# Kernel tuning notes

Measured on AMD Instinct MI355X. Metric: run time of the kernel, lower is better.

Reference implementation:

```python
import jax, jax.numpy as jnp
import numpy as np

B, S, R = 1, 128, 384          # batch, n_seq (MSA rows), n_res
C_M, C_Z, H, D = 256, 128, 8, 32  # msa channels, pair channels, heads, head dim


def layernorm(x, g, b, eps=1e-5):
    mu = jnp.mean(x, axis=-1, keepdims=True)
    var = jnp.var(x, axis=-1, keepdims=True)
    return (x - mu) * jax.lax.rsqrt(var + eps) * g + b


def setup_inputs() -> dict:
    key = jax.random.key(0)
    ks = jax.random.split(key, 10)
    w = lambda k, shape: jax.random.normal(k, shape, jnp.float32) * 0.02
    return {
        "msa_act": jax.random.normal(ks[0], (B, S, R, C_M), jnp.float32),
        "pair_act": jax.random.normal(ks[1], (B, R, R, C_Z), jnp.float32),
        "msa_mask": jnp.ones((B, S, R), jnp.float32),
        "qn_g": jnp.ones((C_M,), jnp.float32),
        "qn_b": jnp.zeros((C_M,), jnp.float32),
        "pn_g": jnp.ones((C_Z,), jnp.float32),
        "pn_b": jnp.zeros((C_Z,), jnp.float32),
        "w_pair": w(ks[2], (C_Z, H)),           # feat_2d_weights (no bias)
        "wq": w(ks[3], (C_M, H, D)),
        "wk": w(ks[4], (C_M, H, D)),
        "wv": w(ks[5], (C_M, H, D)),
        "wg": w(ks[6], (C_M, H, D)),            # gating linear
        "bg": jnp.ones((H, D), jnp.float32),     # gating bias (AF2 inits to 1)
        "wo": w(ks[7], (H, D, C_M)),             # output projection
        "bo": jnp.zeros((C_M,), jnp.float32),
    }


def reference(msa_act, pair_act, msa_mask, qn_g, qn_b, pn_g, pn_b,
              w_pair, wq, wk, wv, wg, bg, wo, bo):
    # pair bias: LN + Linear(c_z -> H), -> [B, 1, H, R, R]
    z = jnp.einsum('bijc,ch->bhij', layernorm(pair_act, pn_g, pn_b), w_pair)[:, None]
    # mask bias: [B, S, 1, 1, R]
    mask_bias = (1e9 * (msa_mask - 1.0))[:, :, None, None, :]

    m = layernorm(msa_act, qn_g, qn_b)
    q = jnp.einsum('bsrc,chd->bshrd', m, wq) * (D ** -0.5)
    k = jnp.einsum('bsrc,chd->bshrd', m, wk)
    v = jnp.einsum('bsrc,chd->bshrd', m, wv)

    logits = jnp.einsum('bshqd,bshkd->bshqk', q, k) + mask_bias + z  # [B,S,H,R,R]
    a = jax.nn.softmax(logits, axis=-1)
    o = jnp.einsum('bshqk,bshkd->bsqhd', a, v)                       # [B,S,R,H,D]

    g = jax.nn.sigmoid(jnp.einsum('bsrc,chd->bsrhd', m, wg) + bg)
    out = jnp.einsum('bsrhd,hdc->bsrc', o * g, wo) + bo              # [B,S,R,C_M]
    return out
```

## Files before the change

### kernel.cpp

```cpp
#include <hip/hip_runtime.h>
#include <hip/hip_bf16.h>

typedef unsigned int uint;
typedef unsigned short ushortT;
typedef __attribute__((ext_vector_type(8))) short bf16x8;
typedef __attribute__((ext_vector_type(4))) float f32x4;

#define S_ 128
#define R_ 384
#define CM 256
#define CZ 128
#define H_ 8
#define D_ 32
#define SR (S_*R_)
#define RRTOT (R_*R_)
#define SHRD (S_*H_*R_*D_)

__device__ __forceinline__ float bf2f(ushortT u) {
    return __uint_as_float(((uint)u) << 16);
}
__device__ __forceinline__ ushortT f2bf(float f) {
    uint x = __float_as_uint(f);
    x += 0x7FFFu + ((x >> 16) & 1u);
    return (ushortT)(x >> 16);
}
__device__ __forceinline__ uint pack_bf2(float lo, float hi) {
    return (uint)f2bf(lo) | ((uint)f2bf(hi) << 16);
}

__global__ __launch_bounds__(256) void k_prep(
        const float* __restrict__ wq, const float* __restrict__ wk,
        const float* __restrict__ wv, const float* __restrict__ wg,
        const float* __restrict__ wo,
        ushortT* __restrict__ wt, ushortT* __restrict__ wgt,
        ushortT* __restrict__ wot) {
    int id = blockIdx.x * 256 + threadIdx.x;
    int which = id >> 16, r16 = id & 65535;
    int y = r16 & 255, x = r16 >> 8;
    if (which == 0)      wt[(size_t)y*256 + x]       = f2bf(wq[(size_t)x*256 + y] * 0.17677669529663687f);
    else if (which == 1) wt[(size_t)(256+y)*256 + x] = f2bf(wk[(size_t)x*256 + y]);
    else if (which == 2) wt[(size_t)(512+y)*256 + x] = f2bf(wv[(size_t)x*256 + y]);
    else if (which == 3) wgt[(size_t)y*256 + x]      = f2bf(wg[(size_t)x*256 + y]);
    else                 wot[(size_t)y*256 + x]      = f2bf(wo[(size_t)x*256 + y]);
}

__global__ __launch_bounds__(256) void k_pair_bias(
        const float* __restrict__ pair, const float* __restrict__ pn_g,
        const float* __restrict__ pn_b, const float* __restrict__ w_pair,
        ushortT* __restrict__ z) {
    int wave = threadIdx.x >> 6, lane = threadIdx.x & 63;
    int row = blockIdx.x * 4 + wave;
    const float* x = pair + (size_t)row * CZ;
    float2 xv = *(const float2*)&x[lane * 2];
    float s  = xv.x + xv.y;
    float s2 = xv.x*xv.x + xv.y*xv.y;
    #pragma unroll
    for (int off = 32; off; off >>= 1) {
        s  += __shfl_xor(s,  off);
        s2 += __shfl_xor(s2, off);
    }
    float mu  = s * (1.0f / 128.0f);
    float var = s2 * (1.0f / 128.0f) - mu * mu;
    float rstd = rsqrtf(var + 1e-5f);
    float2 gv = *(const float2*)&pn_g[lane * 2];
    float2 bv = *(const float2*)&pn_b[lane * 2];
    float n0 = (xv.x - mu) * rstd * gv.x + bv.x;
    float n1 = (xv.y - mu) * rstd * gv.y + bv.y;
    float4 wa = *(const float4*)&w_pair[lane*16     ];
    float4 wb = *(const float4*)&w_pair[lane*16 +  4];
    float4 wc = *(const float4*)&w_pair[lane*16 +  8];
    float4 wd = *(const float4*)&w_pair[lane*16 + 12];
    float v0_ = n0*wa.x + n1*wc.x, v1_ = n0*wa.y + n1*wc.y;
    float v2_ = n0*wa.z + n1*wc.z, v3_ = n0*wa.w + n1*wc.w;
    float v4_ = n0*wb.x + n1*wd.x, v5_ = n0*wb.y + n1*wd.y;
    float v6_ = n0*wb.z + n1*wd.z, v7_ = n0*wb.w + n1*wd.w;
    float x0 = __shfl_xor(v0_,1), x1 = __shfl_xor(v1_,1), x2 = __shfl_xor(v2_,1), x3 = __shfl_xor(v3_,1);
    float x4 = __shfl_xor(v4_,1), x5 = __shfl_xor(v5_,1), x6 = __shfl_xor(v6_,1), x7 = __shfl_xor(v7_,1);
    bool b0 = (lane & 1) != 0;
    float u0 = b0 ? v4_+x4 : v0_+x0;
    float u1 = b0 ? v5_+x5 : v1_+x1;
    float u2 = b0 ? v6_+x6 : v2_+x2;
    float u3 = b0 ? v7_+x7 : v3_+x3;
    float y0 = __shfl_xor(u0,2), y1 = __shfl_xor(u1,2), y2 = __shfl_xor(u2,2), y3 = __shfl_xor(u3,2);
    bool b1 = (lane & 2) != 0;
    float w0 = b1 ? u2+y2 : u0+y0;
    float w1 = b1 ? u3+y3 : u1+y1;
    float z0 = __shfl_xor(w0,4), z1 = __shfl_xor(w1,4);
    bool b2 = (lane & 4) != 0;
    float val = b2 ? w1+z1 : w0+z0;
    val += __shfl_xor(val, 8);
    val += __shfl_xor(val, 16);
    val += __shfl_xor(val, 32);
    int hmap = 4*(lane & 1) + 2*((lane >> 1) & 1) + ((lane >> 2) & 1);
    if (lane < 8) z[(size_t)hmap * RRTOT + row] = f2bf(val);
}

__device__ __forceinline__ void ln_row_f4(
        const float* __restrict__ src, const float* __restrict__ gam,
        const float* __restrict__ bet, char* msb, int row, int lane) {
    float4 xv = *(const float4*)&src[lane * 4];
    float sm = (xv.x + xv.y) + (xv.z + xv.w);
    float s2 = (xv.x*xv.x + xv.y*xv.y) + (xv.z*xv.z + xv.w*xv.w);
    #pragma unroll
    for (int off = 32; off; off >>= 1) {
        sm += __shfl_xor(sm, off);
        s2 += __shfl_xor(s2, off);
    }
    float mu  = sm * (1.0f / 256.0f);
    float var = s2 * (1.0f / 256.0f) - mu * mu;
    float rstd = rsqrtf(var + 1e-5f);
    float4 gv = *(const float4*)&gam[lane * 4];
    float4 bv = *(const float4*)&bet[lane * 4];
    float n0 = (xv.x - mu) * rstd * gv.x + bv.x, n1 = (xv.y - mu) * rstd * gv.y + bv.y;
    float n2 = (xv.z - mu) * rstd * gv.z + bv.z, n3 = (xv.w - mu) * rstd * gv.w + bv.w;
    uint2 w; w.x = pack_bf2(n0, n1); w.y = pack_bf2(n2, n3);
    *(uint2*)(msb + ((row*512 + lane*8) ^ ((row & 7) << 4))) = w;
}

__global__ __launch_bounds__(256) void k_msa_qkv(
        const float* __restrict__ msa, const float* __restrict__ qn_g,
        const float* __restrict__ qn_b, const ushortT* __restrict__ wt,
        ushortT* __restrict__ qo, ushortT* __restrict__ ko,
        ushortT* __restrict__ vto) {
    __shared__ ushortT m_sh[32 * 256];
    __shared__ ushortT st_sh[3 * 32 * 256];
    int tid = threadIdx.x, wave = tid >> 6, lane = tid & 63;
    int c = lane & 15, g = (lane >> 4) & 3;
    int r0 = blockIdx.x * 32, s = r0 / R_, rl0 = r0 % R_;
    char* msb = (char*)m_sh;
    char* stb = (char*)st_sh;

    #pragma unroll
    for (int i = 0; i < 8; ++i) {
        int row = wave * 8 + i;
        ln_row_f4(msa + (size_t)(r0 + row) * CM, qn_g, qn_b, msb, row, lane);
    }
    __syncthreads();

    bf16x8 af[2][8];
    #pragma unroll
    for (int rt = 0; rt < 2; ++rt)
        #pragma unroll
        for (int kc = 0; kc < 8; ++kc) {
            int row = rt*16 + c;
            af[rt][kc] = *(const bf16x8*)(msb + ((row*512 + (kc*32 + 8*g)*2) ^ ((c & 7) << 4)));
        }

    const f32x4 z4 = {0.f, 0.f, 0.f, 0.f};
    #pragma unroll
    for (int mI = 0; mI < 3; ++mI) {
        char* osb = stb + mI * 16384;
        int tb = wave * 4;
        const ushortT* wb0 = wt + ((size_t)(mI*256 + tb*16 + c)) * 256 + 8*g;
        const ushortT* wb1 = wb0 + 16*256;
        const ushortT* wb2 = wb0 + 32*256;
        const ushortT* wb3 = wb0 + 48*256;
        f32x4 a0L = z4, a0H = z4, a1L = z4, a1H = z4;
        f32x4 a2L = z4, a2H = z4, a3L = z4, a3H = z4;
        #pragma unroll
        for (int kc = 0; kc < 8; ++kc) {
            bf16x8 b0 = *(const bf16x8*)(wb0 + kc*32);
            bf16x8 b1 = *(const bf16x8*)(wb1 + kc*32);
            bf16x8 b2 = *(const bf16x8*)(wb2 + kc*32);
            bf16x8 b3 = *(const bf16x8*)(wb3 + kc*32);
            a0L = __builtin_amdgcn_mfma_f32_16x16x32_bf16(af[0][kc], b0, a0L, 0, 0, 0);
            a0H = __builtin_amdgcn_mfma_f32_16x16x32_bf16(af[1][kc], b0, a0H, 0, 0, 0);
            a1L = __builtin_amdgcn_mfma_f32_16x16x32_bf16(af[0][kc], b1, a1L, 0, 0, 0);
            a1H = __builtin_amdgcn_mfma_f32_16x16x32_bf16(af[1][kc], b1, a1H, 0, 0, 0);
            a2L = __builtin_amdgcn_mfma_f32_16x16x32_bf16(af[0][kc], b2, a2L, 0, 0, 0);
            a2H = __builtin_amdgcn_mfma_f32_16x16x32_bf16(af[1][kc], b2, a2H, 0, 0, 0);
            a3L = __builtin_amdgcn_mfma_f32_16x16x32_bf16(af[0][kc], b3, a3L, 0, 0, 0);
            a3H = __builtin_amdgcn_mfma_f32_16x16x32_bf16(af[1][kc], b3, a3H, 0, 0, 0);
        }
        #pragma unroll
        for (int j = 0; j < 4; ++j) {
            f32x4 lo = (j == 0) ? a0L : (j == 1) ? a1L : (j == 2) ? a2L : a3L;
            f32x4 hi = (j == 0) ? a0H : (j == 1) ? a1H : (j == 2) ? a2H : a3H;
            if (mI < 2) {
                int col = (tb + j)*16 + c;
                #pragma unroll
                for (int r = 0; r < 4; ++r) {
                    int row0 = 4*g + r, row1 = row0 + 16;
                    *(ushortT*)(osb + ((row0*512 + col*2) ^ ((row0 & 7) << 4))) = f2bf(lo[r]);
                    *(ushortT*)(osb + ((row1*512 + col*2) ^ ((row1 & 7) << 4))) = f2bf(hi[r]);
                }
            } else {
                int hd = (tb + j)*16 + c;
                #pragma unroll
                for (int r = 0; r < 4; ++r) {
                    int rlo = 4*g + r, rhi = rlo + 16;
                    *(ushortT*)(osb + ((hd*64 + rlo*2) ^ ((hd & 3) << 4))) = f2bf(lo[r]);
                    *(ushortT*)(osb + ((hd*64 + rhi*2) ^ ((hd & 3) << 4))) = f2bf(hi[r]);
                }
            }
        }
    }
    __syncthreads();

    #pragma unroll
    for (int m = 0; m < 2; ++m) {
        char* osb = stb + m * 16384;
        ushortT* O = (m == 0) ? qo : ko;
        #pragma unroll
        for (int i = 0; i < 4; ++i) {
            int idx = tid + i*256;
            int row = idx >> 5, c16 = idx & 31;
            uint4 vd = *(const uint4*)(osb + ((row*512 + c16*16) ^ ((row & 7) << 4)));
            int hh = c16 >> 2, dq = (c16 & 3) * 8;
            size_t ga = ((size_t)(s*H_ + hh) * R_ + rl0 + row) * D_ + dq;
            *(uint4*)&O[ga] = vd;
        }
    }
    {
        char* osb = stb + 2 * 16384;
        #pragma unroll
        for (int i = 0; i < 4; ++i) {
            int idx = tid + i*256;
            int hd = idx >> 2, q8 = idx & 3;
            uint4 vd = *(const uint4*)(osb + ((hd*64 + q8*16) ^ ((hd & 3) << 4)));
            size_t ga = ((size_t)(s*256 + hd)) * R_ + rl0 + q8*8;
            *(uint4*)&vto[ga] = vd;
        }
    }
}

__global__ __launch_bounds__(512) void k_attn(
        const ushortT* __restrict__ qws, const ushortT* __restrict__ kws,
        const ushortT* __restrict__ vtws, const ushortT* __restrict__ zws,
        const float* __restrict__ mask, float* __restrict__ out) {
    __shared__ ushortT k_sh[R_ * 40];
    __shared__ ushortT vt_sh[D_ * R_];
    __shared__ float   mb[R_];
    __shared__ ushortT p_sh[8 * 1280];
    int tid = threadIdx.x, wave = tid >> 6, lane = tid & 63;
    int c = lane & 15, g = (lane >> 4) & 3;
    int s = blockIdx.x >> 3, h = blockIdx.x & 7;
    size_t base = (size_t)(s * H_ + h) * R_ * D_;

    {
        const uint4* ks = (const uint4*)(kws + base);
        char* kb_ = (char*)k_sh;
        for (int i = tid; i < 1536; i += 512) {
            int row = i >> 2, part = i & 3;
            *(uint4*)(kb_ + row*80 + part*16) = ks[i];
        }
        const uint4* vs = (const uint4*)(vtws + base);
        char* vb = (char*)vt_sh;
        for (int i = tid; i < 1536; i += 512) {
            int d = i / 48, ch = i % 48;
            *(uint4*)(vb + ((d*768 + ch*16) ^ ((d & 7) << 4))) = vs[i];
        }
        for (int j = tid; j < R_; j += 512) mb[j] = 1e9f * (mask[s*R_ + j] - 1.0f);
    }
    __syncthreads();

    const char* ksb = (const char*)k_sh;
    const char* vtb = (const char*)vt_sh;
    char* psb = (char*)p_sh + wave * 2560;
    const f32x4 zero4 = {0.f, 0.f, 0.f, 0.f};

    for (int qt = wave; qt < 24; qt += 8) {
        int q0 = qt * 16;
        bf16x8 qf = *(const bf16x8*)(qws + base + (size_t)(q0 + c) * D_ + 8*g);
        const ushortT* zq = zws + (size_t)h * RRTOT + (size_t)(q0 + c) * R_ + 4*g;

        float sm = 0.f;
        f32x4 o0 = zero4, o1 = zero4;
        #pragma unroll 2
        for (int kb = 0; kb < 12; ++kb) {
            bf16x8 kfA = *(const bf16x8*)(ksb + ((2*kb    )*16 + c)*80 + 16*g);
            bf16x8 kfB = *(const bf16x8*)(ksb + ((2*kb + 1)*16 + c)*80 + 16*g);
            f32x4 pA = __builtin_amdgcn_mfma_f32_16x16x32_bf16(kfA, qf, zero4, 0, 0, 0);
            f32x4 pB = __builtin_amdgcn_mfma_f32_16x16x32_bf16(kfB, qf, zero4, 0, 0, 0);
            float4 mvA = *(const float4*)&mb[(2*kb    )*16 + 4*g];
            float4 mvB = *(const float4*)&mb[(2*kb + 1)*16 + 4*g];
            ushort4 zvA = *(const ushort4*)(zq + (2*kb    )*16);
            ushort4 zvB = *(const ushort4*)(zq + (2*kb + 1)*16);
            pA.x = __expf(pA.x + mvA.x + bf2f(zvA.x));
            pA.y = __expf(pA.y + mvA.y + bf2f(zvA.y));
            pA.z = __expf(pA.z + mvA.z + bf2f(zvA.z));
            pA.w = __expf(pA.w + mvA.w + bf2f(zvA.w));
            pB.x = __expf(pB.x + mvB.x + bf2f(zvB.x));
            pB.y = __expf(pB.y + mvB.y + bf2f(zvB.y));
            pB.z = __expf(pB.z + mvB.z + bf2f(zvB.z));
            pB.w = __expf(pB.w + mvB.w + bf2f(zvB.w));
            sm += (pA.x + pA.y) + (pA.z + pA.w) + (pB.x + pB.y) + (pB.z + pB.w);
            uint2 wA; wA.x = pack_bf2(pA.x, pA.y); wA.y = pack_bf2(pA.z, pA.w);
            uint2 wB; wB.x = pack_bf2(pB.x, pB.y); wB.y = pack_bf2(pB.z, pB.w);
            *(uint2*)(psb + (kb&1)*1280 + c*80 +      8*g) = wA;
            *(uint2*)(psb + (kb&1)*1280 + c*80 + 32 + 8*g) = wB;
            bf16x8 pa = *(const bf16x8*)(psb + (kb&1)*1280 + c*80 + 16*g);
            bf16x8 v0 = *(const bf16x8*)(vtb + (((c     )*768 + kb*64 + 16*g) ^ ((c & 7) << 4)));
            bf16x8 v1 = *(const bf16x8*)(vtb + (((16 + c)*768 + kb*64 + 16*g) ^ ((c & 7) << 4)));
            o0 = __builtin_amdgcn_mfma_f32_16x16x32_bf16(v0, pa, o0, 0, 0, 0);
            o1 = __builtin_amdgcn_mfma_f32_16x16x32_bf16(v1, pa, o1, 0, 0, 0);
        }
        sm += __shfl_xor(sm, 16);
        sm += __shfl_xor(sm, 32);
        float inv = 1.0f / sm;
        float4 s0, s1;
        s0.x = o0[0]*inv; s0.y = o0[1]*inv; s0.z = o0[2]*inv; s0.w = o0[3]*inv;
        s1.x = o1[0]*inv; s1.y = o1[1]*inv; s1.z = o1[2]*inv; s1.w = o1[3]*inv;
        float* ob = out + (size_t)(s*R_ + q0 + c) * CM + h*D_ + 4*g;
        *(float4*)ob = s0;
        *(float4*)(ob + 16) = s1;
    }
}

__global__ __launch_bounds__(256) void k_out(
        const float* __restrict__ msa, const float* __restrict__ qn_g,
        const float* __restrict__ qn_b, const ushortT* __restrict__ wgt,
        const float* __restrict__ bg, const ushortT* __restrict__ wot,
        const float* __restrict__ bo, float* __restrict__ out) {
    __shared__ ushortT m_sh[32 * 256];
    __shared__ ushortT og_sh[32 * 256];
    int tid = threadIdx.x, wave = tid >> 6, lane = tid & 63;
    int c = lane & 15, g = (lane >> 4) & 3;
    int r0 = blockIdx.x * 32;
    char* msb = (char*)m_sh;
    char* ogb = (char*)og_sh;

    #pragma unroll
    for (int i = 0; i < 8; ++i) {
        int row = wave * 8 + i;
        ln_row_f4(msa + (size_t)(r0 + row) * CM, qn_g, qn_b, msb, row, lane);
    }
    __syncthreads();

    bf16x8 af[2][8];
    #pragma unroll
    for (int rt = 0; rt < 2; ++rt)
        #pragma unroll
        for (int kc = 0; kc < 8; ++kc) {
            int row = rt*16 + c;
            af[rt][kc] = *(const bf16x8*)(msb + ((row*512 + (kc*32 + 8*g)*2) ^ ((c & 7) << 4)));
        }

    const f32x4 z4 = {0.f, 0.f, 0.f, 0.f};
    {
        int tb = wave * 4;
        const ushortT* wb0 = wgt + (size_t)(tb*16 + c) * 256 + 8*g;
        const ushortT* wb1 = wb0 + 16*256;
        const ushortT* wb2 = wb0 + 32*256;
        const ushortT* wb3 = wb0 + 48*256;
        f32x4 a0L = z4, a0H = z4, a1L = z4, a1H = z4;
        f32x4 a2L = z4, a2H = z4, a3L = z4, a3H = z4;
        #pragma unroll
        for (int kc = 0; kc < 8; ++kc) {
            bf16x8 b0 = *(const bf16x8*)(wb0 + kc*32);
            bf16x8 b1 = *(const bf16x8*)(wb1 + kc*32);
            bf16x8 b2 = *(const bf16x8*)(wb2 + kc*32);
            bf16x8 b3 = *(const bf16x8*)(wb3 + kc*32);
            a0L = __builtin_amdgcn_mfma_f32_16x16x32_bf16(af[0][kc], b0, a0L, 0, 0, 0);
            a0H = __builtin_amdgcn_mfma_f32_16x16x32_bf16(af[1][kc], b0, a0H, 0, 0, 0);
            a1L = __builtin_amdgcn_mfma_f32_16x16x32_bf16(af[0][kc], b1, a1L, 0, 0, 0);
            a1H = __builtin_amdgcn_mfma_f32_16x16x32_bf16(af[1][kc], b1, a1H, 0, 0, 0);
            a2L = __builtin_amdgcn_mfma_f32_16x16x32_bf16(af[0][kc], b2, a2L, 0, 0, 0);
            a2H = __builtin_amdgcn_mfma_f32_16x16x32_bf16(af[1][kc], b2, a2H, 0, 0, 0);
            a3L = __builtin_amdgcn_mfma_f32_16x16x32_bf16(af[0][kc], b3, a3L, 0, 0, 0);
            a3H = __builtin_amdgcn_mfma_f32_16x16x32_bf16(af[1][kc], b3, a3H, 0, 0, 0);
        }
        #pragma unroll
        for (int j = 0; j < 4; ++j) {
            f32x4 lo = (j == 0) ? a0L : (j == 1) ? a1L : (j == 2) ? a2L : a3L;
            f32x4 hi = (j == 0) ? a0H : (j == 1) ? a1H : (j == 2) ? a2H : a3H;
            int t = (tb + j)*16 + c;
            float bgv = bg[t];
            #pragma unroll
            for (int r = 0; r < 4; ++r) {
                int row0 = 4*g + r, row1 = row0 + 16;
                float g0 = 1.0f / (1.0f + __expf(-(lo[r] + bgv)));
                float g1 = 1.0f / (1.0f + __expf(-(hi[r] + bgv)));
                float ov0 = out[(size_t)(r0 + row0) * CM + t];
                float ov1 = out[(size_t)(r0 + row1) * CM + t];
                *(ushortT*)(ogb + ((row0*512 + t*2) ^ ((row0 & 7) << 4))) = f2bf(ov0 * g0);
                *(ushortT*)(ogb + ((row1*512 + t*2) ^ ((row1 & 7) << 4))) = f2bf(ov1 * g1);
            }
        }
    }
    __syncthreads();

    bf16x8 af2[2][8];
    #pragma unroll
    for (int rt = 0; rt < 2; ++rt)
        #pragma unroll
        for (int kc = 0; kc < 8; ++kc) {
            int row = rt*16 + c;
            af2[rt][kc] = *(const bf16x8*)(ogb + ((row*512 + (kc*32 + 8*g)*2) ^ ((c & 7) << 4)));
        }

    {
        int tb = wave * 4;
        const ushortT* wb0 = wot + (size_t)(tb*16 + c) * 256 + 8*g;
        const ushortT* wb1 = wb0 + 16*256;
        const ushortT* wb2 = wb0 + 32*256;
        const ushortT* wb3 = wb0 + 48*256;
        f32x4 a0L = z4, a0H = z4, a1L = z4, a1H = z4;
        f32x4 a2L = z4, a2H = z4, a3L = z4, a3H = z4;
        #pragma unroll
        for (int kc = 0; kc < 8; ++kc) {
            bf16x8 b0 = *(const bf16x8*)(wb0 + kc*32);
            bf16x8 b1 = *(const bf16x8*)(wb1 + kc*32);
            bf16x8 b2 = *(const bf16x8*)(wb2 + kc*32);
            bf16x8 b3 = *(const bf16x8*)(wb3 + kc*32);
            a0L = __builtin_amdgcn_mfma_f32_16x16x32_bf16(af2[0][kc], b0, a0L, 0, 0, 0);
            a0H = __builtin_amdgcn_mfma_f32_16x16x32_bf16(af2[1][kc], b0, a0H, 0, 0, 0);
            a1L = __builtin_amdgcn_mfma_f32_16x16x32_bf16(af2[0][kc], b1, a1L, 0, 0, 0);
            a1H = __builtin_amdgcn_mfma_f32_16x16x32_bf16(af2[1][kc], b1, a1H, 0, 0, 0);
            a2L = __builtin_amdgcn_mfma_f32_16x16x32_bf16(af2[0][kc], b2, a2L, 0, 0, 0);
            a2H = __builtin_amdgcn_mfma_f32_16x16x32_bf16(af2[1][kc], b2, a2H, 0, 0, 0);
            a3L = __builtin_amdgcn_mfma_f32_16x16x32_bf16(af2[0][kc], b3, a3L, 0, 0, 0);
            a3H = __builtin_amdgcn_mfma_f32_16x16x32_bf16(af2[1][kc], b3, a3H, 0, 0, 0);
        }
        #pragma unroll
        for (int j = 0; j < 4; ++j) {
            f32x4 lo = (j == 0) ? a0L : (j == 1) ? a1L : (j == 2) ? a2L : a3L;
            f32x4 hi = (j == 0) ? a0H : (j == 1) ? a1H : (j == 2) ? a2H : a3H;
            int t = (tb + j)*16 + c;
            float bov = bo[t];
            #pragma unroll
            for (int r = 0; r < 4; ++r) {
                int row0 = 4*g + r, row1 = row0 + 16;
                out[(size_t)(r0 + row0) * CM + t] = lo[r] + bov;
                out[(size_t)(r0 + row1) * CM + t] = hi[r] + bov;
            }
        }
    }
}

extern "C" void kernel_launch(void* const* d_in, const int* in_sizes, int n_in,
                              void* d_out, int out_size, void* d_ws, size_t ws_size,
                              hipStream_t stream) {
    const float* msa    = (const float*)d_in[0];
    const float* pair   = (const float*)d_in[1];
    const float* mask   = (const float*)d_in[2];
    const float* qn_g   = (const float*)d_in[3];
    const float* qn_b   = (const float*)d_in[4];
    const float* pn_g   = (const float*)d_in[5];
    const float* pn_b   = (const float*)d_in[6];
    const float* w_pair = (const float*)d_in[7];
    const float* wq     = (const float*)d_in[8];
    const float* wk     = (const float*)d_in[9];
    const float* wv     = (const float*)d_in[10];
    const float* wg     = (const float*)d_in[11];
    const float* bg     = (const float*)d_in[12];
    const float* wo     = (const float*)d_in[13];
    const float* bo     = (const float*)d_in[14];
    float* out = (float*)d_out;

    ushortT* qws  = (ushortT*)d_ws;
    ushortT* kws  = qws + (size_t)SHRD;
    ushortT* vtws = kws + (size_t)SHRD;
    ushortT* zws  = vtws + (size_t)SHRD;
    ushortT* wt   = zws + (size_t)H_ * RRTOT;
    ushortT* wgt  = wt + 3 * 65536;
    ushortT* wot  = wgt + 65536;

    k_prep     <<<1280,    256, 0, stream>>>(wq, wk, wv, wg, wo, wt, wgt, wot);
    k_pair_bias<<<RRTOT/4, 256, 0, stream>>>(pair, pn_g, pn_b, w_pair, zws);
    k_msa_qkv  <<<SR/32,   256, 0, stream>>>(msa, qn_g, qn_b, wt, qws, kws, vtws);
    k_attn     <<<S_*H_,   512, 0, stream>>>(qws, kws, vtws, zws, mask, out);
    k_out      <<<SR/32,   256, 0, stream>>>(msa, qn_g, qn_b, wgt, bg, wot, bo, out);
}
```

Baseline: 273.8 us.

## Compute MSA layernorm once into bf16 workspace and share across QKV and output kernels

Adds a standalone layernorm kernel that normalizes the fp32 MSA activations once and writes them as bf16 to a workspace buffer. The QKV and gating/output kernels then load the normalized rows straight from global memory into MFMA fragments, instead of each rereading the fp32 input, recomputing the layernorm and staging it through LDS. This cuts one full fp32 read of the 50MB input and the duplicated layernorm work, at the cost of an extra launch plus a bf16 write and two bf16 reads. The fragment loads are now unswizzled strided global reads. The MFMA loop is also folded into a macro.

```diff
diff --git a/kernel.cpp b/kernel.cpp
--- a/kernel.cpp
+++ b/kernel.cpp
@@ -95,10 +95,7 @@
     if (lane < 8) z[(size_t)hmap * RRTOT + row] = f2bf(val);
 }
 
-__device__ __forceinline__ void ln_row_f4(
-        const float* __restrict__ src, const float* __restrict__ gam,
-        const float* __restrict__ bet, char* msb, int row, int lane) {
-    float4 xv = *(const float4*)&src[lane * 4];
+__device__ __forceinline__ uint2 ln_reduce(float4 xv, float4 gv, float4 bv) {
     float sm = (xv.x + xv.y) + (xv.z + xv.w);
     float s2 = (xv.x*xv.x + xv.y*xv.y) + (xv.z*xv.z + xv.w*xv.w);
     #pragma unroll
@@ -109,42 +106,55 @@
     float mu  = sm * (1.0f / 256.0f);
     float var = s2 * (1.0f / 256.0f) - mu * mu;
     float rstd = rsqrtf(var + 1e-5f);
-    float4 gv = *(const float4*)&gam[lane * 4];
-    float4 bv = *(const float4*)&bet[lane * 4];
-    float n0 = (xv.x - mu) * rstd * gv.x + bv.x, n1 = (xv.y - mu) * rstd * gv.y + bv.y;
-    float n2 = (xv.z - mu) * rstd * gv.z + bv.z, n3 = (xv.w - mu) * rstd * gv.w + bv.w;
-    uint2 w; w.x = pack_bf2(n0, n1); w.y = pack_bf2(n2, n3);
-    *(uint2*)(msb + ((row*512 + lane*8) ^ ((row & 7) << 4))) = w;
-}
-
-__global__ __launch_bounds__(256) void k_msa_qkv(
+    uint2 w;
+    w.x = pack_bf2((xv.x - mu)*rstd*gv.x + bv.x, (xv.y - mu)*rstd*gv.y + bv.y);
+    w.y = pack_bf2((xv.z - mu)*rstd*gv.z + bv.z, (xv.w - mu)*rstd*gv.w + bv.w);
+    return w;
+}
+
+__global__ __launch_bounds__(256) void k_ln(
         const float* __restrict__ msa, const float* __restrict__ qn_g,
-        const float* __restrict__ qn_b, const ushortT* __restrict__ wt,
+        const float* __restrict__ qn_b, ushortT* __restrict__ m) {
+    int wave = threadIdx.x >> 6, lane = threadIdx.x & 63;
+    int r0 = blockIdx.x * 32 + wave * 8;
+    const float* src = msa + (size_t)r0 * CM + lane * 4;
+    float4 x0 = *(const float4*)(src        );
+    float4 x1 = *(const float4*)(src + 1*CM );
+    float4 x2 = *(const float4*)(src + 2*CM );
+    float4 x3 = *(const float4*)(src + 3*CM );
+    float4 x4 = *(const float4*)(src + 4*CM );
+    float4 x5 = *(const float4*)(src + 5*CM );
+    float4 x6 = *(const float4*)(src + 6*CM );
+    float4 x7 = *(const float4*)(src + 7*CM );
+    float4 gv = *(const float4*)&qn_g[lane*4];
+    float4 bv = *(const float4*)&qn_b[lane*4];
+    ushortT* dst = m + (size_t)r0 * CM + lane * 4;
+    *(uint2*)(dst       ) = ln_reduce(x0, gv, bv);
+    *(uint2*)(dst + 1*CM) = ln_reduce(x1, gv, bv);
+    *(uint2*)(dst + 2*CM) = ln_reduce(x2, gv, bv);
+    *(uint2*)(dst + 3*CM) = ln_reduce(x3, gv, bv);
+    *(uint2*)(dst + 4*CM) = ln_reduce(x4, gv, bv);
+    *(uint2*)(dst + 5*CM) = ln_reduce(x5, gv, bv);
+    *(uint2*)(dst + 6*CM) = ln_reduce(x6, gv, bv);
+    *(uint2*)(dst + 7*CM) = ln_reduce(x7, gv, bv);
+}
+
+__global__ __launch_bounds__(256) void k_msa_qkv_m(
+        const ushortT* __restrict__ m, const ushortT* __restrict__ wt,
         ushortT* __restrict__ qo, ushortT* __restrict__ ko,
         ushortT* __restrict__ vto) {
-    __shared__ ushortT m_sh[32 * 256];
     __shared__ ushortT st_sh[3 * 32 * 256];
     int tid = threadIdx.x, wave = tid >> 6, lane = tid & 63;
     int c = lane & 15, g = (lane >> 4) & 3;
     int r0 = blockIdx.x * 32, s = r0 / R_, rl0 = r0 % R_;
-    char* msb = (char*)m_sh;
     char* stb = (char*)st_sh;
 
-    #pragma unroll
-    for (int i = 0; i < 8; ++i) {
-        int row = wave * 8 + i;
-        ln_row_f4(msa + (size_t)(r0 + row) * CM, qn_g, qn_b, msb, row, lane);
-    }
-    __syncthreads();
-
     bf16x8 af[2][8];
     #pragma unroll
     for (int rt = 0; rt < 2; ++rt)
         #pragma unroll
-        for (int kc = 0; kc < 8; ++kc) {
-            int row = rt*16 + c;
-            af[rt][kc] = *(const bf16x8*)(msb + ((row*512 + (kc*32 + 8*g)*2) ^ ((c & 7) << 4)));
-        }
+        for (int kc = 0; kc < 8; ++kc)
+            af[rt][kc] = *(const bf16x8*)(m + (size_t)(r0 + rt*16 + c) * CM + kc*32 + 8*g);
 
     const f32x4 z4 = {0.f, 0.f, 0.f, 0.f};
     #pragma unroll
@@ -198,9 +208,9 @@
     __syncthreads();
 
     #pragma unroll
-    for (int m = 0; m < 2; ++m) {
-        char* osb = stb + m * 16384;
-        ushortT* O = (m == 0) ? qo : ko;
+    for (int mm = 0; mm < 2; ++mm) {
+        char* osb = stb + mm * 16384;
+        ushortT* O = (mm == 0) ? qo : ko;
         #pragma unroll
         for (int i = 0; i < 4; ++i) {
             int idx = tid + i*256;
@@ -307,59 +317,49 @@
     }
 }
 
-__global__ __launch_bounds__(256) void k_out(
-        const float* __restrict__ msa, const float* __restrict__ qn_g,
-        const float* __restrict__ qn_b, const ushortT* __restrict__ wgt,
+#define MFMA_GROUP4(AF, WB)                                                          \
+    {                                                                                \
+        _Pragma("unroll")                                                            \
+        for (int kc = 0; kc < 8; ++kc) {                                             \
+            bf16x8 b0 = *(const bf16x8*)((WB) + kc*32);                              \
+            bf16x8 b1 = *(const bf16x8*)((WB) + 16*256 + kc*32);                     \
+            bf16x8 b2 = *(const bf16x8*)((WB) + 32*256 + kc*32);                     \
+            bf16x8 b3 = *(const bf16x8*)((WB) + 48*256 + kc*32);                     \
+            a0L = __builtin_amdgcn_mfma_f32_16x16x32_bf16(AF[0][kc], b0, a0L, 0,0,0);\
+            a0H = __builtin_amdgcn_mfma_f32_16x16x32_bf16(AF[1][kc], b0, a0H, 0,0,0);\
+            a1L = __builtin_amdgcn_mfma_f32_16x16x32_bf16(AF[0][kc], b1, a1L, 0,0,0);\
+            a1H = __builtin_amdgcn_mfma_f32_16x16x32_bf16(AF[1][kc], b1, a1H, 0,0,0);\
+            a2L = __builtin_amdgcn_mfma_f32_16x16x32_bf16(AF[0][kc], b2, a2L, 0,0,0);\
+            a2H = __builtin_amdgcn_mfma_f32_16x16x32_bf16(AF[1][kc], b2, a2H, 0,0,0);\
+            a3L = __builtin_amdgcn_mfma_f32_16x16x32_bf16(AF[0][kc], b3, a3L, 0,0,0);\
+            a3H = __builtin_amdgcn_mfma_f32_16x16x32_bf16(AF[1][kc], b3, a3H, 0,0,0);\
+        }                                                                            \
+    }
+
+__global__ __launch_bounds__(256) void k_out_m(
+        const ushortT* __restrict__ m, const ushortT* __restrict__ wgt,
         const float* __restrict__ bg, const ushortT* __restrict__ wot,
         const float* __restrict__ bo, float* __restrict__ out) {
-    __shared__ ushortT m_sh[32 * 256];
     __shared__ ushortT og_sh[32 * 256];
     int tid = threadIdx.x, wave = tid >> 6, lane = tid & 63;
     int c = lane & 15, g = (lane >> 4) & 3;
     int r0 = blockIdx.x * 32;
-    char* msb = (char*)m_sh;
     char* ogb = (char*)og_sh;
 
-    #pragma unroll
-    for (int i = 0; i < 8; ++i) {
-        int row = wave * 8 + i;
-        ln_row_f4(msa + (size_t)(r0 + row) * CM, qn_g, qn_b, msb, row, lane);
-    }
-    __syncthreads();
-
     bf16x8 af[2][8];
     #pragma unroll
     for (int rt = 0; rt < 2; ++rt)
         #pragma unroll
-        for (int kc = 0; kc < 8; ++kc) {
-            int row = rt*16 + c;
-            af[rt][kc] = *(const bf16x8*)(msb + ((row*512 + (kc*32 + 8*g)*2) ^ ((c & 7) << 4)));
-        }
+        for (int kc = 0; kc < 8; ++kc)
+            af[rt][kc] = *(const bf16x8*)(m + (size_t)(r0 + rt*16 + c) * CM + kc*32 + 8*g);
 
     const f32x4 z4 = {0.f, 0.f, 0.f, 0.f};
     {
         int tb = wave * 4;
         const ushortT* wb0 = wgt + (size_t)(tb*16 + c) * 256 + 8*g;
-        const ushortT* wb1 = wb0 + 16*256;
-        const ushortT* wb2 = wb0 + 32*256;
-        const ushortT* wb3 = wb0 + 48*256;
         f32x4 a0L = z4, a0H = z4, a1L = z4, a1H = z4;
         f32x4 a2L = z4, a2H = z4, a3L = z4, a3H = z4;
-        #pragma unroll
-        for (int kc = 0; kc < 8; ++kc) {
-            bf16x8 b0 = *(const bf16x8*)(wb0 + kc*32);
-            bf16x8 b1 = *(const bf16x8*)(wb1 + kc*32);
-            bf16x8 b2 = *(const bf16x8*)(wb2 + kc*32);
-            bf16x8 b3 = *(const bf16x8*)(wb3 + kc*32);
-            a0L = __builtin_amdgcn_mfma_f32_16x16x32_bf16(af[0][kc], b0, a0L, 0, 0, 0);
-            a0H = __builtin_amdgcn_mfma_f32_16x16x32_bf16(af[1][kc], b0, a0H, 0, 0, 0);
-            a1L = __builtin_amdgcn_mfma_f32_16x16x32_bf16(af[0][kc], b1, a1L, 0, 0, 0);
-            a1H = __builtin_amdgcn_mfma_f32_16x16x32_bf16(af[1][kc], b1, a1H, 0, 0, 0);
-            a2L = __builtin_amdgcn_mfma_f32_16x16x32_bf16(af[0][kc], b2, a2L, 0, 0, 0);
-            a2H = __builtin_amdgcn_mfma_f32_16x16x32_bf16(af[1][kc], b2, a2H, 0, 0, 0);
-            a3L = __builtin_amdgcn_mfma_f32_16x16x32_bf16(af[0][kc], b3, a3L, 0, 0, 0);
-            a3H = __builtin_amdgcn_mfma_f32_16x16x32_bf16(af[1][kc], b3, a3H, 0, 0, 0);
-        }
+        MFMA_GROUP4(af, wb0);
         #pragma unroll
         for (int j = 0; j < 4; ++j) {
             f32x4 lo = (j == 0) ? a0L : (j == 1) ? a1L : (j == 2) ? a2L : a3L;
@@ -392,26 +392,9 @@
     {
         int tb = wave * 4;
         const ushortT* wb0 = wot + (size_t)(tb*16 + c) * 256 + 8*g;
-        const ushortT* wb1 = wb0 + 16*256;
-        const ushortT* wb2 = wb0 + 32*256;
-        const ushortT* wb3 = wb0 + 48*256;
         f32x4 a0L = z4, a0H = z4, a1L = z4, a1H = z4;
         f32x4 a2L = z4, a2H = z4, a3L = z4, a3H = z4;
-        #pragma unroll
-        for (int kc = 0; kc < 8; ++kc) {
-            bf16x8 b0 = *(const bf16x8*)(wb0 + kc*32);
-            bf16x8 b1 = *(const bf16x8*)(wb1 + kc*32);
-            bf16x8 b2 = *(const bf16x8*)(wb2 + kc*32);
-            bf16x8 b3 = *(const bf16x8*)(wb3 + kc*32);
-            a0L = __builtin_amdgcn_mfma_f32_16x16x32_bf16(af2[0][kc], b0, a0L, 0, 0, 0);
-            a0H = __builtin_amdgcn_mfma_f32_16x16x32_bf16(af2[1][kc], b0, a0H, 0, 0, 0);
-            a1L = __builtin_amdgcn_mfma_f32_16x16x32_bf16(af2[0][kc], b1, a1L, 0, 0, 0);
-            a1H = __builtin_amdgcn_mfma_f32_16x16x32_bf16(af2[1][kc], b1, a1H, 0, 0, 0);
-            a2L = __builtin_amdgcn_mfma_f32_16x16x32_bf16(af2[0][kc], b2, a2L, 0, 0, 0);
-            a2H = __builtin_amdgcn_mfma_f32_16x16x32_bf16(af2[1][kc], b2, a2H, 0, 0, 0);
-            a3L = __builtin_amdgcn_mfma_f32_16x16x32_bf16(af2[0][kc], b3, a3L, 0, 0, 0);
-            a3H = __builtin_amdgcn_mfma_f32_16x16x32_bf16(af2[1][kc], b3, a3H, 0, 0, 0);
-        }
+        MFMA_GROUP4(af2, wb0);
         #pragma unroll
         for (int j = 0; j < 4; ++j) {
             f32x4 lo = (j == 0) ? a0L : (j == 1) ? a1L : (j == 2) ? a2L : a3L;
@@ -455,10 +438,12 @@
     ushortT* wt   = zws + (size_t)H_ * RRTOT;
     ushortT* wgt  = wt + 3 * 65536;
     ushortT* wot  = wgt + 65536;
-
-    k_prep     <<<1280,    256, 0, stream>>>(wq, wk, wv, wg, wo, wt, wgt, wot);
-    k_pair_bias<<<RRTOT/4, 256, 0, stream>>>(pair, pn_g, pn_b, w_pair, zws);
-    k_msa_qkv  <<<SR/32,   256, 0, stream>>>(msa, qn_g, qn_b, wt, qws, kws, vtws);
-    k_attn     <<<S_*H_,   512, 0, stream>>>(qws, kws, vtws, zws, mask, out);
-    k_out      <<<SR/32,   256, 0, stream>>>(msa, qn_g, qn_b, wgt, bg, wot, bo, out);
-}
+    ushortT* mws  = wot + 65536;
+
+    k_prep      <<<1280,    256, 0, stream>>>(wq, wk, wv, wg, wo, wt, wgt, wot);
+    k_pair_bias <<<RRTOT/4, 256, 0, stream>>>(pair, pn_g, pn_b, w_pair, zws);
+    k_ln        <<<SR/32,   256, 0, stream>>>(msa, qn_g, qn_b, mws);
+    k_msa_qkv_m <<<SR/32,   256, 0, stream>>>(mws, wt, qws, kws, vtws);
+    k_attn      <<<S_*H_,   512, 0, stream>>>(qws, kws, vtws, zws, mask, out);
+    k_out_m     <<<SR/32,   256, 0, stream>>>(mws, wgt, bg, wot, bo, out);
+}
```

Result: slower. 291.2 us (+6.3%).
